# Performance work log

Hardware: AMD Instinct MI355X
Metric: run time of the kernel (lower is better)

Reference implementation:

```python
import jax, jax.numpy as jnp
import numpy as np
import math

D_INPUT = 1024
D_Q = 1024
D_K = 1024
D_V = 1024
D_MODEL = 1024
B, S = 4, 2048


def setup_inputs() -> dict:
    key = jax.random.key(0)
    ks = jax.random.split(key, 9)
    sc = 0.02
    return {
        "x": jax.random.normal(ks[0], (B, S, D_INPUT), dtype=jnp.float32),
        "wq": jax.random.normal(ks[1], (D_INPUT, D_Q), dtype=jnp.float32) * sc,
        "bq": jnp.zeros((D_Q,), dtype=jnp.float32),
        "wk": jax.random.normal(ks[2], (D_INPUT, D_K), dtype=jnp.float32) * sc,
        "bk": jnp.zeros((D_K,), dtype=jnp.float32),
        "wv": jax.random.normal(ks[3], (D_INPUT, D_V), dtype=jnp.float32) * sc,
        "bv": jnp.zeros((D_V,), dtype=jnp.float32),
        "wp": jax.random.normal(ks[4], (D_V, D_MODEL), dtype=jnp.float32) * sc,
        "bp": jnp.zeros((D_MODEL,), dtype=jnp.float32),
    }


def reference(x, wq, bq, wk, bk, wv, bv, wp, bp):
    scale = math.sqrt(D_K)  # NOTE: original MULTIPLIES by sqrt(d_k)
    q = x @ wq + bq  # [B,S,Dq]
    k = x @ wk + bk  # [B,S,Dk]
    v = x @ wv + bv  # [B,S,Dv]
    scores = jnp.einsum('bsd,btd->bst', q, k) * scale
    p_attn = jax.nn.softmax(scores, axis=-1)
    # dropout: inference mode (training=False) -> identity
    context = jnp.einsum('bst,btd->bsd', p_attn, v)
    output = context @ wp + bp
    return (output, p_attn)
```

## Files before the change

kernel.cpp:

```cpp
#include <hip/hip_runtime.h>

typedef unsigned short u16;
typedef short bf16x8 __attribute__((ext_vector_type(8)));
typedef float floatx4 __attribute__((ext_vector_type(4)));

static __device__ __forceinline__ u16 f2bf(float f) {
  unsigned int u = __float_as_uint(f);
  unsigned int lsb = (u >> 16) & 1u;
  u += 0x7FFFu + lsb;
  return (u16)(u >> 16);
}
static __device__ __forceinline__ float bf2f(u16 u) {
  return __uint_as_float(((unsigned int)u) << 16);
}

static __device__ __forceinline__ void gl_lds16(const u16* g, u16* l) {
  __builtin_amdgcn_global_load_lds(
      (const __attribute__((address_space(1))) void*)g,
      (__attribute__((address_space(3))) void*)l, 16, 0, 0);
}

__global__ __launch_bounds__(256)
void prep_weights(const float* __restrict__ wq, const float* __restrict__ wk,
                  const float* __restrict__ wv, const float* __restrict__ wp,
                  u16* __restrict__ qkThi, u16* __restrict__ qkTlo,
                  u16* __restrict__ wvThi, u16* __restrict__ wpThi) {
  __shared__ float t[32][33];
  const int z = blockIdx.z;
  const float* in = (z == 0) ? wq : (z == 1) ? wk : (z == 2) ? wv : wp;
  u16* hi = (z == 0) ? qkThi : (z == 1) ? (qkThi + 1024 * 1024)
           : (z == 2) ? wvThi : wpThi;
  u16* lo = (z == 0) ? qkTlo : (z == 1) ? (qkTlo + 1024 * 1024) : (u16*)nullptr;
  const int want_lo = (z < 2);

  const int r0 = blockIdx.y * 32, c0 = blockIdx.x * 32;
  const int tid = threadIdx.x;
  const int lr = tid >> 3;
  const int lc = (tid & 7) * 4;
  float4 v = *(const float4*)(in + (size_t)(r0 + lr) * 1024 + c0 + lc);
  t[lr][lc + 0] = v.x; t[lr][lc + 1] = v.y; t[lr][lc + 2] = v.z; t[lr][lc + 3] = v.w;
  __syncthreads();
  u16 ph[4], pl[4];
#pragma unroll
  for (int j = 0; j < 4; j++) {
    float f = t[lc + j][lr];
    ph[j] = f2bf(f);
    pl[j] = f2bf(f - bf2f(ph[j]));
  }
  const size_t o = (size_t)(c0 + lr) * 1024 + r0 + lc;
  *(uint2*)(hi + o) = *(uint2*)ph;
  if (want_lo) *(uint2*)(lo + o) = *(uint2*)pl;
}

__global__ __launch_bounds__(256)
void concat_bias(const float* __restrict__ bq, const float* __restrict__ bk,
                 float* __restrict__ out) {
  const int i = blockIdx.x * 256 + threadIdx.x;
  out[i] = (i < 1024) ? bq[i] : bk[i - 1024];
}

__global__ __launch_bounds__(256)
void split_f32(const float* __restrict__ in, u16* __restrict__ hi,
               u16* __restrict__ lo) {
  const size_t i4 = ((size_t)blockIdx.x * 256 + threadIdx.x) * 4;
  float4 v = *(const float4*)(in + i4);
  float f[4] = {v.x, v.y, v.z, v.w};
  u16 ph[4], pl[4];
#pragma unroll
  for (int j = 0; j < 4; j++) {
    ph[j] = f2bf(f[j]);
    pl[j] = f2bf(f[j] - bf2f(ph[j]));
  }
  *(uint2*)(hi + i4) = *(uint2*)ph;
  *(uint2*)(lo + i4) = *(uint2*)pl;
}

template<int A_SPLIT, int B_SPLIT, int OUT_MODE, int HAS_BIAS, int T>
__global__ __launch_bounds__(256)
void gemm_mfma(const u16* __restrict__ Ahi, const u16* __restrict__ Alo,
               const u16* __restrict__ Bhi, const u16* __restrict__ Blo,
               const float* __restrict__ bias,
               void* __restrict__ C0, void* __restrict__ C1,
               int M, int N, int K, int lda, int ldb, int ldc,
               long long aB, long long bB, long long cB, float scale) {
  __shared__ __align__(16) u16 As[(1 + A_SPLIT) * 128 * 32];
  __shared__ __align__(16) u16 Bs[(1 + B_SPLIT) * 128 * 32];

  const int bz = blockIdx.z;
  const u16* A0 = Ahi + (size_t)bz * aB;
  const u16* A1 = A_SPLIT ? (Alo + (size_t)bz * aB) : (const u16*)nullptr;
  const u16* B0 = Bhi + (size_t)bz * bB;
  const u16* B1 = B_SPLIT ? (Blo + (size_t)bz * bB) : (const u16*)nullptr;

  const int m0 = blockIdx.y * 128;
  const int tid = threadIdx.x;
  const int w = tid >> 6;
  const int L = tid & 63;
  const int rr = L & 15, quad = L >> 4;
  const int wm = (w >> 1) * 64, wn = (w & 1) * 64;

  const int c3 = (L & 3) ^ ((L >> 3) & 3);
  const int srow = w * 32 + (L >> 2);
  u16* stA = &As[w * 1024];
  u16* stB = &Bs[w * 1024];
  const u16* gA0 = A0 + (size_t)(m0 + srow) * lda + c3 * 8;
  const u16* gA1 = A_SPLIT ? A1 + (size_t)(m0 + srow) * lda + c3 * 8 : (const u16*)nullptr;

  const int pcb = (quad ^ ((rr >> 1) & 3)) * 8;

  for (int t = 0; t < T; t++) {
    const int n0 = (blockIdx.x * T + t) * 128;
    const u16* gB0 = B0 + (size_t)(n0 + srow) * ldb + c3 * 8;
    const u16* gB1 = B_SPLIT ? B1 + (size_t)(n0 + srow) * ldb + c3 * 8 : (const u16*)nullptr;

    floatx4 acc[4][4] = {};

    for (int k0 = 0; k0 < K; k0 += 32) {
      gl_lds16(gA0 + k0, stA);
      gl_lds16(gA0 + k0 + 16 * (size_t)lda, stA + 512);
      gl_lds16(gB0 + k0, stB);
      gl_lds16(gB0 + k0 + 16 * (size_t)ldb, stB + 512);
      if (A_SPLIT) {
        gl_lds16(gA1 + k0, stA + 4096);
        gl_lds16(gA1 + k0 + 16 * (size_t)lda, stA + 4096 + 512);
      }
      if (B_SPLIT) {
        gl_lds16(gB1 + k0, stB + 4096);
        gl_lds16(gB1 + k0 + 16 * (size_t)ldb, stB + 4096 + 512);
      }
      __syncthreads();

      bf16x8 a0[4], a1[4], b0[4], b1[4];
#pragma unroll
      for (int i = 0; i < 4; i++) {
        const int arow = wm + i * 16 + rr;
        const int brow = wn + i * 16 + rr;
        a0[i] = *(const bf16x8*)&As[arow * 32 + pcb];
        if (A_SPLIT) a1[i] = *(const bf16x8*)&As[4096 + arow * 32 + pcb];
        b0[i] = *(const bf16x8*)&Bs[brow * 32 + pcb];
        if (B_SPLIT) b1[i] = *(const bf16x8*)&Bs[4096 + brow * 32 + pcb];
      }
#pragma unroll
      for (int i = 0; i < 4; i++) {
#pragma unroll
        for (int j = 0; j < 4; j++) {
          acc[i][j] = __builtin_amdgcn_mfma_f32_16x16x32_bf16(a0[i], b0[j], acc[i][j], 0, 0, 0);
          if (A_SPLIT && B_SPLIT) {
            acc[i][j] = __builtin_amdgcn_mfma_f32_16x16x32_bf16(a0[i], b1[j], acc[i][j], 0, 0, 0);
            acc[i][j] = __builtin_amdgcn_mfma_f32_16x16x32_bf16(a1[i], b0[j], acc[i][j], 0, 0, 0);
          }
        }
      }
      __syncthreads();
    }

#pragma unroll
    for (int i = 0; i < 4; i++) {
      const int mbase = m0 + wm + i * 16 + quad * 4;
#pragma unroll
      for (int j = 0; j < 4; j++) {
        const int col = n0 + wn + j * 16 + rr;
        float bvs = 0.f;
        if (HAS_BIAS) bvs = bias[col];
        if (OUT_MODE == 3) {
          u16 pk[4];
#pragma unroll
          for (int ii = 0; ii < 4; ii++) pk[ii] = f2bf(acc[i][j][ii] * scale + bvs);
          const size_t idx = (size_t)(mbase >> 11) * (2048 * 1024) + (size_t)col * 2048 + (mbase & 2047);
          *(uint2*)((u16*)C0 + idx) = *(uint2*)pk;
        } else {
          u16* Cb = (u16*)C0 + (size_t)bz * cB;
          float* Cf = (float*)C0 + (size_t)bz * cB;
          u16* Cl = (OUT_MODE == 1) ? ((u16*)C1 + (size_t)bz * cB) : (u16*)nullptr;
#pragma unroll
          for (int ii = 0; ii < 4; ii++) {
            const float v = acc[i][j][ii] * scale + bvs;
            const size_t idx = (size_t)(mbase + ii) * ldc + col;
            if (OUT_MODE == 0) {
              Cb[idx] = f2bf(v);
            } else if (OUT_MODE == 1) {
              const u16 h = f2bf(v);
              Cb[idx] = h;
              Cl[idx] = f2bf(v - bf2f(h));
            } else if (OUT_MODE == 2) {
              Cf[idx] = v;
            }
          }
        }
      }
    }
  }
}

__global__ __launch_bounds__(256)
void softmax_rows(float* __restrict__ S, u16* __restrict__ Pb) {
  const int row = blockIdx.x;
  float* s = S + (size_t)row * 2048;
  const int tid = threadIdx.x;
  const int w = tid >> 6;
  __shared__ float redm[4];
  __shared__ float reds[4];

  float v[8];
  float mx = -1e30f;
#pragma unroll
  for (int i = 0; i < 8; i++) {
    v[i] = s[tid + 256 * i];
    mx = fmaxf(mx, v[i]);
  }
#pragma unroll
  for (int o = 32; o > 0; o >>= 1) mx = fmaxf(mx, __shfl_xor(mx, o, 64));
  if ((tid & 63) == 0) redm[w] = mx;
  __syncthreads();
  mx = fmaxf(fmaxf(redm[0], redm[1]), fmaxf(redm[2], redm[3]));

  float sum = 0.f;
#pragma unroll
  for (int i = 0; i < 8; i++) {
    v[i] = __expf(v[i] - mx);
    sum += v[i];
  }
#pragma unroll
  for (int o = 32; o > 0; o >>= 1) sum += __shfl_xor(sum, o, 64);
  if ((tid & 63) == 0) reds[w] = sum;
  __syncthreads();
  sum = reds[0] + reds[1] + reds[2] + reds[3];
  const float rs = 1.0f / sum;
#pragma unroll
  for (int i = 0; i < 8; i++) {
    const float p = v[i] * rs;
    s[tid + 256 * i] = p;
    Pb[(size_t)row * 2048 + tid + 256 * i] = f2bf(p);
  }
}

extern "C" void kernel_launch(void* const* d_in, const int* in_sizes, int n_in,
                              void* d_out, int out_size, void* d_ws, size_t ws_size,
                              hipStream_t stream) {
  const float* x  = (const float*)d_in[0];
  const float* wq = (const float*)d_in[1];
  const float* bq = (const float*)d_in[2];
  const float* wk = (const float*)d_in[3];
  const float* bk = (const float*)d_in[4];
  const float* wv = (const float*)d_in[5];
  const float* bv = (const float*)d_in[6];
  const float* wp = (const float*)d_in[7];
  const float* bp = (const float*)d_in[8];

  const size_t MB = 1024 * 1024;
  char* ws = (char*)d_ws;
  u16* qkThi = (u16*)(ws + 0 * MB);
  u16* qkTlo = (u16*)(ws + 4 * MB);
  u16* wvThi = (u16*)(ws + 8 * MB);
  u16* wpThi = (u16*)(ws + 10 * MB);
  float* bqk = (float*)(ws + 12 * MB);
  u16* xhi   = (u16*)(ws + 13 * MB);
  u16* xlo   = (u16*)(ws + 29 * MB);
  u16* qkhi  = (u16*)(ws + 45 * MB);
  u16* qklo  = (u16*)(ws + 77 * MB);
  u16* vT    = (u16*)(ws + 109 * MB);
  u16* pbf   = qklo;
  u16* ctx   = qkhi;

  float* outp = (float*)d_out;
  float* scf  = (float*)d_out + 8388608;

  const dim3 blk(256);

  prep_weights<<<dim3(32, 32, 4), blk, 0, stream>>>(wq, wk, wv, wp,
                                                    qkThi, qkTlo, wvThi, wpThi);
  concat_bias<<<dim3(8), blk, 0, stream>>>(bq, bk, bqk);
  split_f32<<<dim3(8192), blk, 0, stream>>>(x, xhi, xlo);

  gemm_mfma<1, 1, 1, 1, 2><<<dim3(8, 64, 1), blk, 0, stream>>>(
      xhi, xlo, qkThi, qkTlo, bqk, qkhi, qklo,
      8192, 2048, 1024, 1024, 1024, 2048, 0, 0, 0, 1.0f);

  gemm_mfma<0, 0, 3, 1, 1><<<dim3(8, 64, 1), blk, 0, stream>>>(
      xhi, nullptr, wvThi, nullptr, bv, vT, nullptr,
      8192, 1024, 1024, 1024, 1024, 0, 0, 0, 0, 1.0f);

  gemm_mfma<1, 1, 2, 0, 2><<<dim3(8, 16, 4), blk, 0, stream>>>(
      qkhi, qklo, qkhi + 1024, qklo + 1024, nullptr, scf, nullptr,
      2048, 2048, 1024, 2048, 2048, 2048,
      2048LL * 2048, 2048LL * 2048, 2048LL * 2048, 32.0f);

  softmax_rows<<<dim3(8192), blk, 0, stream>>>(scf, pbf);

  gemm_mfma<0, 0, 0, 0, 1><<<dim3(8, 16, 4), blk, 0, stream>>>(
      pbf, nullptr, vT, nullptr, nullptr, ctx, nullptr,
      2048, 1024, 2048, 2048, 2048, 1024,
      2048LL * 2048, 1024LL * 2048, 2048LL * 1024, 1.0f);

  gemm_mfma<0, 0, 2, 1, 1><<<dim3(8, 64, 1), blk, 0, stream>>>(
      ctx, nullptr, wpThi, nullptr, bp, outp, nullptr,
      8192, 1024, 1024, 1024, 1024, 1024, 0, 0, 0, 1.0f);
}
```

Measured before the change: 514.8 us.

## Fuse QKV projection into one GEMM, merge bias prep, add KB=64 tiles

Merges the Q/K and V projection GEMMs into a single launch over 3072 output columns. Only the Q/K column range runs the split-precision 3-MFMA path, and the V columns take the plain bf16 path and are written transposed. The bias concat kernel is folded into prep_weights, and the T loop (two N-tiles per block) is removed, so the grids get wider. The PV and output GEMMs now use a 64-wide K tile with a new swizzle, which halves barrier count per K but uses more LDS. The runtime bsplit branch could add divergence or register pressure.

```diff
diff --git a/kernel.cpp b/kernel.cpp
--- a/kernel.cpp
+++ b/kernel.cpp
@@ -23,18 +23,26 @@
 __global__ __launch_bounds__(256)
 void prep_weights(const float* __restrict__ wq, const float* __restrict__ wk,
                   const float* __restrict__ wv, const float* __restrict__ wp,
-                  u16* __restrict__ qkThi, u16* __restrict__ qkTlo,
-                  u16* __restrict__ wvThi, u16* __restrict__ wpThi) {
+                  const float* __restrict__ bq, const float* __restrict__ bk,
+                  const float* __restrict__ bv,
+                  u16* __restrict__ qkvThi, u16* __restrict__ qkvTlo,
+                  u16* __restrict__ wpThi, float* __restrict__ bqkv) {
   __shared__ float t[32][33];
   const int z = blockIdx.z;
+  const int tid = threadIdx.x;
+  if (z == 4) {
+    if (blockIdx.y == 0 && blockIdx.x < 12) {
+      const int i = blockIdx.x * 256 + tid;
+      bqkv[i] = (i < 1024) ? bq[i] : (i < 2048) ? bk[i - 1024] : bv[i - 2048];
+    }
+    return;
+  }
   const float* in = (z == 0) ? wq : (z == 1) ? wk : (z == 2) ? wv : wp;
-  u16* hi = (z == 0) ? qkThi : (z == 1) ? (qkThi + 1024 * 1024)
-           : (z == 2) ? wvThi : wpThi;
-  u16* lo = (z == 0) ? qkTlo : (z == 1) ? (qkTlo + 1024 * 1024) : (u16*)nullptr;
+  u16* hi = (z == 3) ? wpThi : (qkvThi + (size_t)z * 1024 * 1024);
+  u16* lo = (z == 0) ? qkvTlo : (z == 1) ? (qkvTlo + 1024 * 1024) : (u16*)nullptr;
   const int want_lo = (z < 2);
 
   const int r0 = blockIdx.y * 32, c0 = blockIdx.x * 32;
-  const int tid = threadIdx.x;
   const int lr = tid >> 3;
   const int lc = (tid & 7) * 4;
   float4 v = *(const float4*)(in + (size_t)(r0 + lr) * 1024 + c0 + lc);
@@ -50,13 +58,6 @@
   const size_t o = (size_t)(c0 + lr) * 1024 + r0 + lc;
   *(uint2*)(hi + o) = *(uint2*)ph;
   if (want_lo) *(uint2*)(lo + o) = *(uint2*)pl;
-}
-
-__global__ __launch_bounds__(256)
-void concat_bias(const float* __restrict__ bq, const float* __restrict__ bk,
-                 float* __restrict__ out) {
-  const int i = blockIdx.x * 256 + threadIdx.x;
-  out[i] = (i < 1024) ? bq[i] : bk[i - 1024];
 }
 
 __global__ __launch_bounds__(256)
@@ -75,117 +76,144 @@
   *(uint2*)(lo + i4) = *(uint2*)pl;
 }
 
-template<int A_SPLIT, int B_SPLIT, int OUT_MODE, int HAS_BIAS, int T>
+template<int KB, int ASP, int BSP, int OM, int HB>
 __global__ __launch_bounds__(256)
 void gemm_mfma(const u16* __restrict__ Ahi, const u16* __restrict__ Alo,
                const u16* __restrict__ Bhi, const u16* __restrict__ Blo,
                const float* __restrict__ bias,
                void* __restrict__ C0, void* __restrict__ C1,
-               int M, int N, int K, int lda, int ldb, int ldc,
-               long long aB, long long bB, long long cB, float scale) {
-  __shared__ __align__(16) u16 As[(1 + A_SPLIT) * 128 * 32];
-  __shared__ __align__(16) u16 Bs[(1 + B_SPLIT) * 128 * 32];
+               void* __restrict__ C2, void* __restrict__ C3,
+               void* __restrict__ C4,
+               int N, int K, int lda, int ldb, int ldc,
+               long long aB, long long bB, long long cB, float scale,
+               int nsplit) {
+  constexpr int CM = KB / 8 - 1;
+  constexpr int RPI = 512 / KB;
+  constexpr int NI = KB / 16;
+  constexpr int PL = 128 * KB;
+  __shared__ __align__(16) u16 As[(1 + ASP) * PL];
+  __shared__ __align__(16) u16 Bs[(1 + BSP) * PL];
 
   const int bz = blockIdx.z;
   const u16* A0 = Ahi + (size_t)bz * aB;
-  const u16* A1 = A_SPLIT ? (Alo + (size_t)bz * aB) : (const u16*)nullptr;
+  const u16* A1 = ASP ? (Alo + (size_t)bz * aB) : (const u16*)nullptr;
   const u16* B0 = Bhi + (size_t)bz * bB;
-  const u16* B1 = B_SPLIT ? (Blo + (size_t)bz * bB) : (const u16*)nullptr;
+  const u16* B1 = BSP ? (Blo + (size_t)bz * bB) : (const u16*)nullptr;
 
   const int m0 = blockIdx.y * 128;
+  const int n0 = blockIdx.x * 128;
+  const bool bsplit = (ASP && BSP) ? (n0 < nsplit) : false;
   const int tid = threadIdx.x;
   const int w = tid >> 6;
   const int L = tid & 63;
   const int rr = L & 15, quad = L >> 4;
   const int wm = (w >> 1) * 64, wn = (w & 1) * 64;
 
-  const int c3 = (L & 3) ^ ((L >> 3) & 3);
-  const int srow = w * 32 + (L >> 2);
-  u16* stA = &As[w * 1024];
-  u16* stB = &Bs[w * 1024];
+  const int lrow = (KB == 32) ? (L >> 2) : (L >> 3);
+  const int c3 = (L & CM) ^ ((L >> 3) & CM);
+  const int srow = w * 32 + lrow;
+  u16* stA = &As[w * 32 * KB];
+  u16* stB = &Bs[w * 32 * KB];
   const u16* gA0 = A0 + (size_t)(m0 + srow) * lda + c3 * 8;
-  const u16* gA1 = A_SPLIT ? A1 + (size_t)(m0 + srow) * lda + c3 * 8 : (const u16*)nullptr;
-
-  const int pcb = (quad ^ ((rr >> 1) & 3)) * 8;
-
-  for (int t = 0; t < T; t++) {
-    const int n0 = (blockIdx.x * T + t) * 128;
-    const u16* gB0 = B0 + (size_t)(n0 + srow) * ldb + c3 * 8;
-    const u16* gB1 = B_SPLIT ? B1 + (size_t)(n0 + srow) * ldb + c3 * 8 : (const u16*)nullptr;
-
-    floatx4 acc[4][4] = {};
-
-    for (int k0 = 0; k0 < K; k0 += 32) {
-      gl_lds16(gA0 + k0, stA);
-      gl_lds16(gA0 + k0 + 16 * (size_t)lda, stA + 512);
-      gl_lds16(gB0 + k0, stB);
-      gl_lds16(gB0 + k0 + 16 * (size_t)ldb, stB + 512);
-      if (A_SPLIT) {
-        gl_lds16(gA1 + k0, stA + 4096);
-        gl_lds16(gA1 + k0 + 16 * (size_t)lda, stA + 4096 + 512);
-      }
-      if (B_SPLIT) {
-        gl_lds16(gB1 + k0, stB + 4096);
-        gl_lds16(gB1 + k0 + 16 * (size_t)ldb, stB + 4096 + 512);
-      }
-      __syncthreads();
-
+  const u16* gA1 = ASP ? A1 + (size_t)(m0 + srow) * lda + c3 * 8 : (const u16*)nullptr;
+  const u16* gB0 = B0 + (size_t)(n0 + srow) * ldb + c3 * 8;
+  const u16* gB1 = BSP ? B1 + (size_t)(n0 + srow) * ldb + c3 * 8 : (const u16*)nullptr;
+
+  floatx4 acc[4][4] = {};
+
+  for (int k0 = 0; k0 < K; k0 += KB) {
+#pragma unroll
+    for (int q = 0; q < NI; q++) {
+      gl_lds16(gA0 + k0 + (size_t)q * RPI * lda, stA + q * 512);
+      gl_lds16(gB0 + k0 + (size_t)q * RPI * ldb, stB + q * 512);
+    }
+    if (ASP && bsplit) {
+#pragma unroll
+      for (int q = 0; q < NI; q++)
+        gl_lds16(gA1 + k0 + (size_t)q * RPI * lda, stA + PL + q * 512);
+    }
+    if (BSP && bsplit) {
+#pragma unroll
+      for (int q = 0; q < NI; q++)
+        gl_lds16(gB1 + k0 + (size_t)q * RPI * ldb, stB + PL + q * 512);
+    }
+    __syncthreads();
+
+#pragma unroll
+    for (int s = 0; s < KB / 32; s++) {
+      const int pcb = (KB == 32) ? (quad ^ ((rr >> 1) & 3)) * 8
+                                 : ((s * 4 + quad) ^ (rr & 7)) * 8;
       bf16x8 a0[4], a1[4], b0[4], b1[4];
 #pragma unroll
       for (int i = 0; i < 4; i++) {
         const int arow = wm + i * 16 + rr;
         const int brow = wn + i * 16 + rr;
-        a0[i] = *(const bf16x8*)&As[arow * 32 + pcb];
-        if (A_SPLIT) a1[i] = *(const bf16x8*)&As[4096 + arow * 32 + pcb];
-        b0[i] = *(const bf16x8*)&Bs[brow * 32 + pcb];
-        if (B_SPLIT) b1[i] = *(const bf16x8*)&Bs[4096 + brow * 32 + pcb];
-      }
-#pragma unroll
-      for (int i = 0; i < 4; i++) {
-#pragma unroll
-        for (int j = 0; j < 4; j++) {
-          acc[i][j] = __builtin_amdgcn_mfma_f32_16x16x32_bf16(a0[i], b0[j], acc[i][j], 0, 0, 0);
-          if (A_SPLIT && B_SPLIT) {
-            acc[i][j] = __builtin_amdgcn_mfma_f32_16x16x32_bf16(a0[i], b1[j], acc[i][j], 0, 0, 0);
-            acc[i][j] = __builtin_amdgcn_mfma_f32_16x16x32_bf16(a1[i], b0[j], acc[i][j], 0, 0, 0);
+        a0[i] = *(const bf16x8*)&As[arow * KB + pcb];
+        b0[i] = *(const bf16x8*)&Bs[brow * KB + pcb];
+        if (ASP && BSP) {
+          if (bsplit) {
+            a1[i] = *(const bf16x8*)&As[PL + arow * KB + pcb];
+            b1[i] = *(const bf16x8*)&Bs[PL + brow * KB + pcb];
           }
         }
       }
-      __syncthreads();
-    }
-
-#pragma unroll
-    for (int i = 0; i < 4; i++) {
-      const int mbase = m0 + wm + i * 16 + quad * 4;
-#pragma unroll
-      for (int j = 0; j < 4; j++) {
-        const int col = n0 + wn + j * 16 + rr;
-        float bvs = 0.f;
-        if (HAS_BIAS) bvs = bias[col];
-        if (OUT_MODE == 3) {
-          u16 pk[4];
-#pragma unroll
-          for (int ii = 0; ii < 4; ii++) pk[ii] = f2bf(acc[i][j][ii] * scale + bvs);
-          const size_t idx = (size_t)(mbase >> 11) * (2048 * 1024) + (size_t)col * 2048 + (mbase & 2047);
-          *(uint2*)((u16*)C0 + idx) = *(uint2*)pk;
-        } else {
-          u16* Cb = (u16*)C0 + (size_t)bz * cB;
-          float* Cf = (float*)C0 + (size_t)bz * cB;
-          u16* Cl = (OUT_MODE == 1) ? ((u16*)C1 + (size_t)bz * cB) : (u16*)nullptr;
-#pragma unroll
-          for (int ii = 0; ii < 4; ii++) {
-            const float v = acc[i][j][ii] * scale + bvs;
-            const size_t idx = (size_t)(mbase + ii) * ldc + col;
-            if (OUT_MODE == 0) {
-              Cb[idx] = f2bf(v);
-            } else if (OUT_MODE == 1) {
-              const u16 h = f2bf(v);
-              Cb[idx] = h;
-              Cl[idx] = f2bf(v - bf2f(h));
-            } else if (OUT_MODE == 2) {
-              Cf[idx] = v;
+#pragma unroll
+      for (int i = 0; i < 4; i++) {
+#pragma unroll
+        for (int j = 0; j < 4; j++) {
+          acc[i][j] = __builtin_amdgcn_mfma_f32_16x16x32_bf16(a0[i], b0[j], acc[i][j], 0, 0, 0);
+          if (ASP && BSP) {
+            if (bsplit) {
+              acc[i][j] = __builtin_amdgcn_mfma_f32_16x16x32_bf16(a0[i], b1[j], acc[i][j], 0, 0, 0);
+              acc[i][j] = __builtin_amdgcn_mfma_f32_16x16x32_bf16(a1[i], b0[j], acc[i][j], 0, 0, 0);
             }
           }
+        }
+      }
+    }
+    __syncthreads();
+  }
+
+#pragma unroll
+  for (int i = 0; i < 4; i++) {
+    const int mbase = m0 + wm + i * 16 + quad * 4;
+#pragma unroll
+    for (int j = 0; j < 4; j++) {
+      const int col = n0 + wn + j * 16 + rr;
+      float bvs = 0.f;
+      if (HB) bvs = bias[col];
+      if (OM == 4) {
+        if (col < 2048) {
+          u16* hi; u16* lo;
+          if (col < 1024) { hi = (u16*)C0; lo = (u16*)C1; }
+          else            { hi = (u16*)C2; lo = (u16*)C3; }
+          const int cc = col & 1023;
+#pragma unroll
+          for (int ii = 0; ii < 4; ii++) {
+            const float v = acc[i][j][ii] + bvs;
+            const size_t idx = (size_t)(mbase + ii) * 1024 + cc;
+            const u16 h = f2bf(v);
+            hi[idx] = h;
+            lo[idx] = f2bf(v - bf2f(h));
+          }
+        } else {
+          const int d = col - 2048;
+          u16 pk[4];
+#pragma unroll
+          for (int ii = 0; ii < 4; ii++) pk[ii] = f2bf(acc[i][j][ii] + bvs);
+          const size_t idx = (size_t)(mbase >> 11) * (2048 * 1024) +
+                             (size_t)d * 2048 + (mbase & 2047);
+          *(uint2*)((u16*)C4 + idx) = *(uint2*)pk;
+        }
+      } else {
+        u16* Cb = (u16*)C0 + (size_t)bz * cB;
+        float* Cf = (float*)C0 + (size_t)bz * cB;
+#pragma unroll
+        for (int ii = 0; ii < 4; ii++) {
+          const float v = acc[i][j][ii] * scale + bvs;
+          const size_t idx = (size_t)(mbase + ii) * ldc + col;
+          if (OM == 0) Cb[idx] = f2bf(v);
+          else         Cf[idx] = v;
         }
       }
     }
@@ -249,50 +277,46 @@
 
   const size_t MB = 1024 * 1024;
   char* ws = (char*)d_ws;
-  u16* qkThi = (u16*)(ws + 0 * MB);
-  u16* qkTlo = (u16*)(ws + 4 * MB);
-  u16* wvThi = (u16*)(ws + 8 * MB);
-  u16* wpThi = (u16*)(ws + 10 * MB);
-  float* bqk = (float*)(ws + 12 * MB);
-  u16* xhi   = (u16*)(ws + 13 * MB);
-  u16* xlo   = (u16*)(ws + 29 * MB);
-  u16* qkhi  = (u16*)(ws + 45 * MB);
-  u16* qklo  = (u16*)(ws + 77 * MB);
-  u16* vT    = (u16*)(ws + 109 * MB);
-  u16* pbf   = qklo;
-  u16* ctx   = qkhi;
+  u16* qkvThi = (u16*)(ws + 0 * MB);
+  u16* qkvTlo = (u16*)(ws + 6 * MB);
+  u16* wpThi  = (u16*)(ws + 10 * MB);
+  float* bqkv = (float*)(ws + 12 * MB);
+  u16* xhi    = (u16*)(ws + 13 * MB);
+  u16* xlo    = (u16*)(ws + 29 * MB);
+  u16* qhi    = (u16*)(ws + 45 * MB);
+  u16* qlo    = (u16*)(ws + 61 * MB);
+  u16* khi    = (u16*)(ws + 77 * MB);
+  u16* klo    = (u16*)(ws + 93 * MB);
+  u16* vT     = (u16*)(ws + 109 * MB);
+  u16* pbf    = khi;
+  u16* ctx    = qhi;
 
   float* outp = (float*)d_out;
   float* scf  = (float*)d_out + 8388608;
 
   const dim3 blk(256);
 
-  prep_weights<<<dim3(32, 32, 4), blk, 0, stream>>>(wq, wk, wv, wp,
-                                                    qkThi, qkTlo, wvThi, wpThi);
-  concat_bias<<<dim3(8), blk, 0, stream>>>(bq, bk, bqk);
+  prep_weights<<<dim3(32, 32, 5), blk, 0, stream>>>(
+      wq, wk, wv, wp, bq, bk, bv, qkvThi, qkvTlo, wpThi, bqkv);
   split_f32<<<dim3(8192), blk, 0, stream>>>(x, xhi, xlo);
 
-  gemm_mfma<1, 1, 1, 1, 2><<<dim3(8, 64, 1), blk, 0, stream>>>(
-      xhi, xlo, qkThi, qkTlo, bqk, qkhi, qklo,
-      8192, 2048, 1024, 1024, 1024, 2048, 0, 0, 0, 1.0f);
-
-  gemm_mfma<0, 0, 3, 1, 1><<<dim3(8, 64, 1), blk, 0, stream>>>(
-      xhi, nullptr, wvThi, nullptr, bv, vT, nullptr,
-      8192, 1024, 1024, 1024, 1024, 0, 0, 0, 0, 1.0f);
-
-  gemm_mfma<1, 1, 2, 0, 2><<<dim3(8, 16, 4), blk, 0, stream>>>(
-      qkhi, qklo, qkhi + 1024, qklo + 1024, nullptr, scf, nullptr,
-      2048, 2048, 1024, 2048, 2048, 2048,
-      2048LL * 2048, 2048LL * 2048, 2048LL * 2048, 32.0f);
+  gemm_mfma<32, 1, 1, 4, 1><<<dim3(24, 64, 1), blk, 0, stream>>>(
+      xhi, xlo, qkvThi, qkvTlo, bqkv, qhi, qlo, khi, klo, vT,
+      3072, 1024, 1024, 1024, 0, 0, 0, 0, 1.0f, 2048);
+
+  gemm_mfma<32, 1, 1, 2, 0><<<dim3(16, 16, 4), blk, 0, stream>>>(
+      qhi, qlo, khi, klo, nullptr, scf, nullptr, nullptr, nullptr, nullptr,
+      2048, 1024, 1024, 1024, 2048,
+      2048LL * 1024, 2048LL * 1024, 2048LL * 2048, 32.0f, 2048);
 
   softmax_rows<<<dim3(8192), blk, 0, stream>>>(scf, pbf);
 
-  gemm_mfma<0, 0, 0, 0, 1><<<dim3(8, 16, 4), blk, 0, stream>>>(
-      pbf, nullptr, vT, nullptr, nullptr, ctx, nullptr,
-      2048, 1024, 2048, 2048, 2048, 1024,
-      2048LL * 2048, 1024LL * 2048, 2048LL * 1024, 1.0f);
-
-  gemm_mfma<0, 0, 2, 1, 1><<<dim3(8, 64, 1), blk, 0, stream>>>(
-      ctx, nullptr, wpThi, nullptr, bp, outp, nullptr,
-      8192, 1024, 1024, 1024, 1024, 1024, 0, 0, 0, 1.0f);
-}
+  gemm_mfma<64, 0, 0, 0, 0><<<dim3(8, 16, 4), blk, 0, stream>>>(
+      pbf, nullptr, vT, nullptr, nullptr, ctx, nullptr, nullptr, nullptr, nullptr,
+      1024, 2048, 2048, 2048, 1024,
+      2048LL * 2048, 1024LL * 2048, 2048LL * 1024, 1.0f, 0);
+
+  gemm_mfma<64, 0, 0, 2, 1><<<dim3(8, 64, 1), blk, 0, stream>>>(
+      ctx, nullptr, wpThi, nullptr, bp, outp, nullptr, nullptr, nullptr, nullptr,
+      1024, 1024, 1024, 1024, 1024, 0, 0, 0, 1.0f, 0);
+}
```

After: 513.1 us. No clear change (-0.3%).
